# Optimization experiments

Measured on AMD Instinct MI355X. Metric: run time of the kernel, lower is better.

Reference implementation:

```python
import jax, jax.numpy as jnp
import numpy as np


def setup_inputs() -> dict:
    key = jax.random.key(0)
    B, H, W = 16, 1024, 1024
    x = jax.random.uniform(key, (B, H, W), dtype=jnp.float32)
    return {"x": x, "bit_depth": 1}


def reference(x, bit_depth):
    # --- reduce_color_depth: quantize via truncating int cast (torch .int()) ---
    scale = 255.0 / (2 ** bit_depth - 1)
    xq = jnp.trunc(x * scale) / scale

    # --- spatial_smoothing: 3x3 median filter with reflect padding ---
    B, H, W = xq.shape
    xp = jnp.pad(xq, ((0, 0), (1, 1), (1, 1)), mode="reflect")  # [B, H+2, W+2]
    # stack the 9 shifted views -> [B, H, W, 9] (same as unfold+view)
    patches = jnp.stack(
        [xp[:, i:i + H, j:j + W] for i in range(3) for j in range(3)], axis=-1
    )
    # odd window (9) -> median is the middle order statistic, matching torch.median
    return jnp.median(patches, axis=-1)
```

## Files before the change

kernel.cpp:

```cpp
#include <hip/hip_runtime.h>
#include <math.h>


constexpr int H = 1024;
constexpr int W = 1024;
constexpr int TX = 64;
constexpr int TY = 16;
constexpr int LDS_W = TX + 2;
constexpr int LDS_H = TY + 2;

#define S2(a, b) { float _mn = fminf(a, b); b = fmaxf(a, b); a = _mn; }

__device__ __forceinline__ float median9(float p0, float p1, float p2,
                                         float p3, float p4, float p5,
                                         float p6, float p7, float p8) {
    S2(p1, p2); S2(p4, p5); S2(p7, p8);
    S2(p0, p1); S2(p3, p4); S2(p6, p7);
    S2(p1, p2); S2(p4, p5); S2(p7, p8);
    S2(p0, p3); S2(p5, p8); S2(p4, p7);
    S2(p3, p6); S2(p1, p4); S2(p2, p5);
    S2(p4, p7); S2(p4, p2); S2(p6, p4);
    S2(p4, p2);
    return p4;
}

__global__ __launch_bounds__(256) void fsq_kernel(const float* __restrict__ x,
                                                  const int* __restrict__ bd,
                                                  float* __restrict__ out) {
    __shared__ float tile[LDS_H][LDS_W];

    const int b  = blockIdx.z;
    const int x0 = blockIdx.x * TX;
    const int y0 = blockIdx.y * TY;
    const int tid = threadIdx.x;

    const float scale = 255.0f / (float)((1 << bd[0]) - 1);

    const float* __restrict__ xb = x + (size_t)b * H * W;

    for (int idx = tid; idx < LDS_H * LDS_W; idx += 256) {
        int ry = idx / LDS_W;
        int rx = idx - ry * LDS_W;
        int gy = y0 - 1 + ry;
        int gx = x0 - 1 + rx;
        gy = (gy < 0) ? -gy : ((gy >= H) ? (2 * H - 2 - gy) : gy);
        gx = (gx < 0) ? -gx : ((gx >= W) ? (2 * W - 2 - gx) : gx);
        float v = xb[(size_t)gy * W + gx];
        tile[ry][rx] = truncf(v * scale) / scale;
    }
    __syncthreads();

    const int tx = tid & 63;
    const int tyBase = (tid >> 6) * 4;

    float* __restrict__ ob = out + (size_t)b * H * W;

    #pragma unroll
    for (int i = 0; i < 4; ++i) {
        const int ty = tyBase + i;
        float p0 = tile[ty    ][tx], p1 = tile[ty    ][tx + 1], p2 = tile[ty    ][tx + 2];
        float p3 = tile[ty + 1][tx], p4 = tile[ty + 1][tx + 1], p5 = tile[ty + 1][tx + 2];
        float p6 = tile[ty + 2][tx], p7 = tile[ty + 2][tx + 1], p8 = tile[ty + 2][tx + 2];
        float m = median9(p0, p1, p2, p3, p4, p5, p6, p7, p8);
        ob[(size_t)(y0 + ty) * W + (x0 + tx)] = m;
    }
}

extern "C" void kernel_launch(void* const* d_in, const int* in_sizes, int n_in,
                              void* d_out, int out_size, void* d_ws, size_t ws_size,
                              hipStream_t stream) {
    const float* x  = (const float*)d_in[0];
    const int*   bd = (const int*)d_in[1];
    float*       out = (float*)d_out;

    const int B = in_sizes[0] / (H * W);
    dim3 grid(W / TX, H / TY, B);
    fsq_kernel<<<grid, 256, 0, stream>>>(x, bd, out);
}
```

Before: 136.0 us.

## Use full-row tiles with float4 I/O and reuse sorted column triples across rows

Each block now covers full 1024-wide rows for 8 output rows. Loads and stores use float4 accesses, and the column reflect halo is handled by storing two extra LDS entries per row. Each thread produces 4 outputs per row. It sorts horizontal triples once per row and reuses them across three vertical windows with a reduced merge network. This cuts ALU work and divides by a multiply instead of a divide. In exchange the halo overhead rises from 18/16 to 10/8 rows, and LDS per block grows to about 40KB, which may limit occupancy.

```diff
diff --git a/kernel.cpp b/kernel.cpp
--- a/kernel.cpp
+++ b/kernel.cpp
@@ -4,19 +4,19 @@
 
 constexpr int H = 1024;
 constexpr int W = 1024;
-constexpr int TX = 64;
-constexpr int TY = 16;
-constexpr int LDS_W = TX + 2;
-constexpr int LDS_H = TY + 2;
+constexpr int TY = 8;
+constexpr int NROWS = TY + 2;
+constexpr int LDSW = 1028;
 
 #define S2(a, b) { float _mn = fminf(a, b); b = fmaxf(a, b); a = _mn; }
 
-__device__ __forceinline__ float median9(float p0, float p1, float p2,
-                                         float p3, float p4, float p5,
-                                         float p6, float p7, float p8) {
-    S2(p1, p2); S2(p4, p5); S2(p7, p8);
-    S2(p0, p1); S2(p3, p4); S2(p6, p7);
-    S2(p1, p2); S2(p4, p5); S2(p7, p8);
+__device__ __forceinline__ void sort3(float& a, float& b, float& c) {
+    S2(a, b); S2(b, c); S2(a, b);
+}
+
+__device__ __forceinline__ float merge9(float p0, float p1, float p2,
+                                        float p3, float p4, float p5,
+                                        float p6, float p7, float p8) {
     S2(p0, p3); S2(p5, p8); S2(p4, p7);
     S2(p3, p6); S2(p1, p4); S2(p2, p5);
     S2(p4, p7); S2(p4, p2); S2(p6, p4);
@@ -25,44 +25,90 @@
 }
 
 __global__ __launch_bounds__(256) void fsq_kernel(const float* __restrict__ x,
-                                                  const int* __restrict__ bd,
+                                                  const int* __restrict__ bdp,
                                                   float* __restrict__ out) {
-    __shared__ float tile[LDS_H][LDS_W];
+    __shared__ float tile[NROWS * LDSW];
 
-    const int b  = blockIdx.z;
-    const int x0 = blockIdx.x * TX;
-    const int y0 = blockIdx.y * TY;
-    const int tid = threadIdx.x;
+    const int t  = threadIdx.x;
+    const int y0 = blockIdx.x * TY;
+    const int b  = blockIdx.y;
 
-    const float scale = 255.0f / (float)((1 << bd[0]) - 1);
+    const float q     = (float)((1 << bdp[0]) - 1);
+    const float scale = 255.0f / q;
+    const float rinv  = q / 255.0f;
 
-    const float* __restrict__ xb = x + (size_t)b * H * W;
+    const size_t base = (size_t)b * H * W;
+    const float* __restrict__ xb = x + base;
+    float* __restrict__ ob       = out + base;
 
-    for (int idx = tid; idx < LDS_H * LDS_W; idx += 256) {
-        int ry = idx / LDS_W;
-        int rx = idx - ry * LDS_W;
-        int gy = y0 - 1 + ry;
-        int gx = x0 - 1 + rx;
-        gy = (gy < 0) ? -gy : ((gy >= H) ? (2 * H - 2 - gy) : gy);
-        gx = (gx < 0) ? -gx : ((gx >= W) ? (2 * W - 2 - gx) : gx);
-        float v = xb[(size_t)gy * W + gx];
-        tile[ry][rx] = truncf(v * scale) / scale;
+    #pragma unroll
+    for (int r = 0; r < NROWS; ++r) {
+        int gy = y0 - 1 + r;
+        gy = (gy < 0) ? 1 : ((gy >= H) ? 2 * H - 2 - gy : gy);
+        const float4 v = *(const float4*)(xb + (size_t)gy * W + 4 * t);
+        float4 qv;
+        qv.x = truncf(v.x * scale) * rinv;
+        qv.y = truncf(v.y * scale) * rinv;
+        qv.z = truncf(v.z * scale) * rinv;
+        qv.w = truncf(v.w * scale) * rinv;
+        *(float4*)(&tile[r * LDSW + 4 * t]) = qv;
+    }
+    if (t < 2 * NROWS) {
+        int r = t >> 1, side = t & 1;
+        int gy = y0 - 1 + r;
+        gy = (gy < 0) ? 1 : ((gy >= H) ? 2 * H - 2 - gy : gy);
+        int gx = side ? 1 : 1022;
+        tile[r * LDSW + 1024 + side] = truncf(xb[(size_t)gy * W + gx] * scale) * rinv;
     }
     __syncthreads();
 
-    const int tx = tid & 63;
-    const int tyBase = (tid >> 6) * 4;
+    const int cL = (t == 0) ? 1025 : (4 * t - 1);
+    const int cR = 4 * t + 4;
 
-    float* __restrict__ ob = out + (size_t)b * H * W;
+    float s0[4][3], s1[4][3], s2[4][3];
+    float v[6];
+
+    auto loadrow = [&](int r, float* vv) {
+        const float* row = &tile[r * LDSW];
+        float4 m = *(const float4*)(row + 4 * t);
+        vv[0] = row[cL];
+        vv[1] = m.x; vv[2] = m.y; vv[3] = m.z; vv[4] = m.w;
+        vv[5] = row[cR];
+    };
+
+    loadrow(0, v);
+    #pragma unroll
+    for (int c = 0; c < 4; ++c) {
+        s0[c][0] = v[c]; s0[c][1] = v[c + 1]; s0[c][2] = v[c + 2];
+        sort3(s0[c][0], s0[c][1], s0[c][2]);
+    }
+    loadrow(1, v);
+    #pragma unroll
+    for (int c = 0; c < 4; ++c) {
+        s1[c][0] = v[c]; s1[c][1] = v[c + 1]; s1[c][2] = v[c + 2];
+        sort3(s1[c][0], s1[c][1], s1[c][2]);
+    }
 
     #pragma unroll
-    for (int i = 0; i < 4; ++i) {
-        const int ty = tyBase + i;
-        float p0 = tile[ty    ][tx], p1 = tile[ty    ][tx + 1], p2 = tile[ty    ][tx + 2];
-        float p3 = tile[ty + 1][tx], p4 = tile[ty + 1][tx + 1], p5 = tile[ty + 1][tx + 2];
-        float p6 = tile[ty + 2][tx], p7 = tile[ty + 2][tx + 1], p8 = tile[ty + 2][tx + 2];
-        float m = median9(p0, p1, p2, p3, p4, p5, p6, p7, p8);
-        ob[(size_t)(y0 + ty) * W + (x0 + tx)] = m;
+    for (int r = 2; r < NROWS; ++r) {
+        loadrow(r, v);
+        #pragma unroll
+        for (int c = 0; c < 4; ++c) {
+            s2[c][0] = v[c]; s2[c][1] = v[c + 1]; s2[c][2] = v[c + 2];
+            sort3(s2[c][0], s2[c][1], s2[c][2]);
+        }
+        float4 o;
+        o.x = merge9(s0[0][0], s0[0][1], s0[0][2], s1[0][0], s1[0][1], s1[0][2], s2[0][0], s2[0][1], s2[0][2]);
+        o.y = merge9(s0[1][0], s0[1][1], s0[1][2], s1[1][0], s1[1][1], s1[1][2], s2[1][0], s2[1][1], s2[1][2]);
+        o.z = merge9(s0[2][0], s0[2][1], s0[2][2], s1[2][0], s1[2][1], s1[2][2], s2[2][0], s2[2][1], s2[2][2]);
+        o.w = merge9(s0[3][0], s0[3][1], s0[3][2], s1[3][0], s1[3][1], s1[3][2], s2[3][0], s2[3][1], s2[3][2]);
+        *(float4*)(ob + (size_t)(y0 + r - 2) * W + 4 * t) = o;
+
+        #pragma unroll
+        for (int c = 0; c < 4; ++c) {
+            #pragma unroll
+            for (int k = 0; k < 3; ++k) { s0[c][k] = s1[c][k]; s1[c][k] = s2[c][k]; }
+        }
     }
 }
 
@@ -74,6 +120,6 @@
     float*       out = (float*)d_out;
 
     const int B = in_sizes[0] / (H * W);
-    dim3 grid(W / TX, H / TY, B);
+    dim3 grid(H / TY, B);
     fsq_kernel<<<grid, 256, 0, stream>>>(x, bd, out);
 }
```

New measurement: 116.0 us. 1.17x faster.
